# Kernel tuning notes

Hardware: AMD Instinct MI355X
Metric: run time of the kernel (lower is better)

Reference implementation:

```python
import jax, jax.numpy as jnp
import numpy as np

N_NODES = 100000
N_EDGES = 3200000
IN_FEATS = 256
N_HIDDEN = 256
N_CLASSES = 40


def setup_inputs() -> dict:
    key = jax.random.key(0)
    ks = jax.random.split(key, 8)
    features = jax.random.normal(ks[0], (N_NODES, IN_FEATS), dtype=jnp.float32)
    src = jax.random.randint(ks[1], (N_EDGES,), 0, N_NODES, dtype=jnp.int64)
    dst = jax.random.randint(ks[2], (N_EDGES,), 0, N_NODES, dtype=jnp.int64)
    # Glorot-ish init scaled down for stability
    W0 = jax.random.normal(ks[3], (IN_FEATS, N_HIDDEN), dtype=jnp.float32) * (1.0 / np.sqrt(IN_FEATS))
    W1 = jax.random.normal(ks[4], (N_HIDDEN, N_HIDDEN), dtype=jnp.float32) * (1.0 / np.sqrt(N_HIDDEN))
    W2 = jax.random.normal(ks[5], (N_HIDDEN, N_CLASSES), dtype=jnp.float32) * (1.0 / np.sqrt(N_HIDDEN))
    b0 = jnp.zeros((N_HIDDEN,), jnp.float32)
    b1 = jnp.zeros((N_HIDDEN,), jnp.float32)
    b2 = jnp.zeros((N_CLASSES,), jnp.float32)
    return {"features": features, "src": src, "dst": dst,
            "W0": W0, "b0": b0, "W1": W1, "b1": b1, "W2": W2, "b2": b2}


def _degree_norms(src, dst, n_nodes):
    ones = jnp.ones(src.shape[0], jnp.float32)
    deg_out = jax.ops.segment_sum(ones, src, num_segments=n_nodes)
    deg_in = jax.ops.segment_sum(ones, dst, num_segments=n_nodes)
    # DGL norm='both': clamp degree to >=1 before rsqrt
    norm_out = jax.lax.rsqrt(jnp.maximum(deg_out, 1.0))  # applied on source side
    norm_in = jax.lax.rsqrt(jnp.maximum(deg_in, 1.0))    # applied on dest side
    return norm_out, norm_in


def _graph_conv(h, src, dst, norm_out, norm_in, W, b, activation):
    # h: [N, Fin]. norm='both': D_in^{-1/2} * A * (D_out^{-1/2} * h) @ W + b
    in_f, out_f = W.shape
    h = h * norm_out[:, None]
    if in_f > out_f:
        # mult weight first to reduce message width (DGL optimization, same math)
        h = h @ W
        agg = jax.ops.segment_sum(h[src], dst, num_segments=h.shape[0])
    else:
        agg = jax.ops.segment_sum(h[src], dst, num_segments=h.shape[0])
        agg = agg @ W
    out = agg * norm_in[:, None] + b
    if activation is not None:
        out = activation(out)
    return out


def reference(features, src, dst, W0, b0, W1, b1, W2, b2):
    n = features.shape[0]
    norm_out, norm_in = _degree_norms(src, dst, n)
    h = _graph_conv(features, src, dst, norm_out, norm_in, W0, b0, jax.nn.relu)
    h = _graph_conv(h, src, dst, norm_out, norm_in, W1, b1, jax.nn.relu)
    h = _graph_conv(h, src, dst, norm_out, norm_in, W2, b2, None)
    return h
```

## Files before the change

### kernel.cpp

```cpp
#include <hip/hip_runtime.h>

#define NN 100000
#define NE 3200000
#define F 256
#define NCLS 40
#define NC 391
#define NBLK_H 256
#define EPB (NE / NBLK_H)
#define CW 25000

using h4 = __attribute__((ext_vector_type(4))) _Float16;
using h8 = __attribute__((ext_vector_type(8))) _Float16;
using f4 = __attribute__((ext_vector_type(4))) float;

__global__ __launch_bounds__(256) void hist_k(const int* __restrict__ src,
                                              const int* __restrict__ dst,
                                              unsigned* __restrict__ pcnt,
                                              unsigned* __restrict__ pcc) {
    __shared__ unsigned hsrc[CW];
    __shared__ unsigned hc[NC];
    int t = threadIdx.x, b = blockIdx.x;
    for (int i = t; i < CW; i += 256) hsrc[i] = 0;
    for (int i = t; i < NC; i += 256) hc[i] = 0;
    __syncthreads();
    int beg = b * EPB, end = beg + EPB;
    for (int e = beg + t; e < end; e += 256) {
        int s = src[e];
        atomicAdd(&hsrc[s >> 2], 1u << (8 * (s & 3)));
        atomicAdd(&hc[dst[e] >> 8], 1u);
    }
    __syncthreads();
    unsigned* pc = pcnt + (size_t)b * CW;
    for (int i = t; i < CW; i += 256) pc[i] = hsrc[i];
    unsigned* pb = pcc + (size_t)b * NC;
    for (int i = t; i < NC; i += 256) pb[i] = hc[i];
}

__global__ void rednout_k(const unsigned* __restrict__ pcnt, float* __restrict__ nout) {
    int w = blockIdx.x * blockDim.x + threadIdx.x;
    if (w >= CW) return;
    unsigned s0 = 0, s1 = 0, s2 = 0, s3 = 0;
    for (int b = 0; b < NBLK_H; b++) {
        unsigned v = pcnt[(size_t)b * CW + w];
        s0 += v & 255u; s1 += (v >> 8) & 255u; s2 += (v >> 16) & 255u; s3 += v >> 24;
    }
    float4 o;
    o.x = rsqrtf(fmaxf((float)s0, 1.f));
    o.y = rsqrtf(fmaxf((float)s1, 1.f));
    o.z = rsqrtf(fmaxf((float)s2, 1.f));
    o.w = rsqrtf(fmaxf((float)s3, 1.f));
    *(float4*)(nout + w * 4) = o;
}

__global__ __launch_bounds__(256) void offsets_k(const unsigned* __restrict__ pcc,
                                                 unsigned* __restrict__ curoff,
                                                 unsigned* __restrict__ totals) {
    __shared__ unsigned sh[256];
    int c = blockIdx.x, t = threadIdx.x;
    unsigned v = pcc[(size_t)t * NC + c];
    sh[t] = v;
    __syncthreads();
    for (int off = 1; off < 256; off <<= 1) {
        unsigned x = (t >= off) ? sh[t - off] : 0;
        __syncthreads();
        sh[t] += x;
        __syncthreads();
    }
    curoff[(size_t)t * NC + c] = sh[t] - v;
    if (t == 255) totals[c] = sh[255];
}

__global__ __launch_bounds__(512) void base_k(const unsigned* __restrict__ totals,
                                              int* __restrict__ cbase) {
    __shared__ unsigned sh[512];
    int t = threadIdx.x;
    unsigned v = (t < NC) ? totals[t] : 0;
    sh[t] = v;
    __syncthreads();
    for (int off = 1; off < 512; off <<= 1) {
        unsigned x = (t >= off) ? sh[t - off] : 0;
        __syncthreads();
        sh[t] += x;
        __syncthreads();
    }
    if (t < NC) cbase[t] = (int)(sh[t] - v);
    if (t == 0) cbase[NC] = NE;
}

__global__ __launch_bounds__(256) void p1scat_k(const int* __restrict__ src,
                                                const int* __restrict__ dst,
                                                const int* __restrict__ cbase,
                                                const unsigned* __restrict__ curoff,
                                                unsigned* __restrict__ ebuf) {
    __shared__ int cur[NC];
    int t = threadIdx.x, b = blockIdx.x;
    for (int i = t; i < NC; i += 256)
        cur[i] = cbase[i] + (int)curoff[(size_t)b * NC + i];
    __syncthreads();
    int beg = b * EPB, end = beg + EPB;
    for (int e = beg + t; e < end; e += 256) {
        int d = dst[e];
        int p = atomicAdd(&cur[d >> 8], 1);
        ebuf[p] = (unsigned)src[e] | ((unsigned)(d & 255) << 17);
    }
}

__global__ __launch_bounds__(256) void p2build_k(const int* __restrict__ cbase,
                                                 const unsigned* __restrict__ ebuf,
                                                 int* __restrict__ csr_src,
                                                 int* __restrict__ row_ptr,
                                                 float* __restrict__ nin) {
    __shared__ int cnt[256], cur[256], sh[256];
    int c = blockIdx.x, t = threadIdx.x;
    int beg = cbase[c], end = cbase[c + 1];
    cnt[t] = 0;
    __syncthreads();
    for (int e = beg + t; e < end; e += 256)
        atomicAdd(&cnt[(ebuf[e] >> 17) & 255], 1);
    __syncthreads();
    int v = cnt[t];
    sh[t] = v;
    __syncthreads();
    for (int off = 1; off < 256; off <<= 1) {
        int x = (t >= off) ? sh[t - off] : 0;
        __syncthreads();
        sh[t] += x;
        __syncthreads();
    }
    int pref = sh[t] - v;
    int node = c * 256 + t;
    if (node <= NN) row_ptr[node] = beg + pref;
    if (node < NN)  nin[node] = rsqrtf(fmaxf((float)v, 1.f));
    cur[t] = pref;
    __syncthreads();
    for (int e = beg + t; e < end; e += 256) {
        unsigned w = ebuf[e];
        int p = atomicAdd(&cur[(w >> 17) & 255], 1);
        csr_src[beg + p] = (int)(w & 0x1FFFFu);
    }
}

__global__ void convfeat_k(const float4* __restrict__ fin, const float* __restrict__ nout,
                           h4* __restrict__ fout, int n4) {
    int i = blockIdx.x * blockDim.x + threadIdx.x;
    if (i < n4) {
        float s = nout[i >> 6];
        float4 v = fin[i];
        h4 o;
        o[0] = (_Float16)(v.x * s);
        o[1] = (_Float16)(v.y * s);
        o[2] = (_Float16)(v.z * s);
        o[3] = (_Float16)(v.w * s);
        fout[i] = o;
    }
}

__global__ void convw_k(const float* __restrict__ W, _Float16* __restrict__ Wt,
                        int ncin, int npad) {
    int i = blockIdx.x * blockDim.x + threadIdx.x;
    if (i < npad * 256) {
        int n = i >> 8, k = i & 255;
        Wt[i] = (n < ncin) ? (_Float16)W[k * ncin + n] : (_Float16)0.0f;
    }
}

__global__ __launch_bounds__(256) void agg256h_k(
        const int* __restrict__ row_ptr, const int* __restrict__ csr_src,
        const _Float16* __restrict__ h, _Float16* __restrict__ agg, int nN) {
    int node = (blockIdx.x * blockDim.x + threadIdx.x) >> 6;
    int lane = threadIdx.x & 63;
    if (node >= nN) return;
    int half = lane >> 5, col = lane & 31;
    int beg = row_ptr[node], end = row_ptr[node + 1];
    f4 a[4][2];
#pragma unroll
    for (int u = 0; u < 4; u++) { a[u][0] = (f4){0,0,0,0}; a[u][1] = (f4){0,0,0,0}; }
    int e = beg;
    for (; e + 7 < end; e += 8) {
        int s[4];
#pragma unroll
        for (int u = 0; u < 4; u++) s[u] = csr_src[e + 2 * u + half];
        h8 v[4];
#pragma unroll
        for (int u = 0; u < 4; u++)
            v[u] = *(const h8*)(h + (size_t)s[u] * F + col * 8);
#pragma unroll
        for (int u = 0; u < 4; u++)
#pragma unroll
            for (int j = 0; j < 8; j++) a[u][j >> 2][j & 3] += (float)v[u][j];
    }
    for (int t = e + half; t < end; t += 2) {
        h8 v = *(const h8*)(h + (size_t)csr_src[t] * F + col * 8);
#pragma unroll
        for (int j = 0; j < 8; j++) a[0][j >> 2][j & 3] += (float)v[j];
    }
    float r[8];
#pragma unroll
    for (int j = 0; j < 8; j++)
        r[j] = (a[0][j >> 2][j & 3] + a[1][j >> 2][j & 3])
             + (a[2][j >> 2][j & 3] + a[3][j >> 2][j & 3]);
#pragma unroll
    for (int j = 0; j < 8; j++) r[j] += __shfl_xor(r[j], 32);
    if (half == 0) {
        h8 o;
#pragma unroll
        for (int j = 0; j < 8; j++) o[j] = (_Float16)r[j];
        *(h8*)(agg + (size_t)node * F + col * 8) = o;
    }
}

__global__ __launch_bounds__(256) void agg64h_k(
        const int* __restrict__ row_ptr, const int* __restrict__ csr_src,
        const _Float16* __restrict__ t3, const float* __restrict__ nin,
        const float* __restrict__ b2, float* __restrict__ out, int nN) {
    int node = (blockIdx.x * blockDim.x + threadIdx.x) >> 6;
    int lane = threadIdx.x & 63;
    if (node >= nN) return;
    int q = lane >> 4, c = lane & 15;
    int beg = row_ptr[node], end = row_ptr[node + 1];
    f4 a0 = {0,0,0,0}, a1 = {0,0,0,0};
    int e = beg;
    for (; e + 7 < end; e += 8) {
        int s0 = csr_src[e + q], s1 = csr_src[e + 4 + q];
        h4 v0 = *(const h4*)(t3 + (size_t)s0 * 64 + c * 4);
        h4 v1 = *(const h4*)(t3 + (size_t)s1 * 64 + c * 4);
#pragma unroll
        for (int j = 0; j < 4; j++) { a0[j] += (float)v0[j]; a1[j] += (float)v1[j]; }
    }
    for (int t = e + q; t < end; t += 4) {
        h4 v = *(const h4*)(t3 + (size_t)csr_src[t] * 64 + c * 4);
#pragma unroll
        for (int j = 0; j < 4; j++) a0[j] += (float)v[j];
    }
    float r[4];
#pragma unroll
    for (int j = 0; j < 4; j++) {
        r[j] = a0[j] + a1[j];
        r[j] += __shfl_xor(r[j], 16);
        r[j] += __shfl_xor(r[j], 32);
    }
    if (lane < 10) {
        float ni = nin[node];
        float4 o;
        o.x = r[0] * ni + b2[lane * 4 + 0];
        o.y = r[1] * ni + b2[lane * 4 + 1];
        o.z = r[2] * ni + b2[lane * 4 + 2];
        o.w = r[3] * ni + b2[lane * 4 + 3];
        *(float4*)(out + (size_t)node * NCLS + lane * 4) = o;
    }
}

template <int NT, int EPI>
__global__ __launch_bounds__(512) void gemm_lds_k(
        const _Float16* __restrict__ A, const _Float16* __restrict__ Wt,
        _Float16* __restrict__ C, int M,
        const float* __restrict__ nin, const float* __restrict__ nout,
        const float* __restrict__ bias) {
    constexpr int COLS = NT * 16;
    __shared__ _Float16 lds[COLS * 256];
    char* ldsb = (char*)lds;

    const int tid  = threadIdx.x;
    const int lane = tid & 63;
    const int w    = tid >> 6;
    const int row0 = blockIdx.x * 128;

#pragma unroll
    for (int i = 0; i < COLS / 16; i++) {
        int idx  = (i * 512 + tid) * 8;
        int byte = idx * 2;
        int row  = byte >> 9;
        int swz  = byte ^ ((row & 7) << 4);
        h8 v = *(const h8*)(Wt + idx);
        *(h8*)(ldsb + swz) = v;
    }

    int arow = row0 + w * 16 + (lane & 15);
    if (arow >= M) arow = M - 1;
    const _Float16* Ap = A + (size_t)arow * 256 + (lane >> 4) * 8;
    h8 areg[8];
#pragma unroll
    for (int i = 0; i < 8; i++) areg[i] = *(const h8*)(Ap + i * 32);

    __syncthreads();

    f4 acc[NT];
#pragma unroll
    for (int n = 0; n < NT; n++) acc[n] = (f4){0.f, 0.f, 0.f, 0.f};

#pragma unroll
    for (int k0 = 0; k0 < 8; k0++) {
        int kb = (k0 * 32 + (lane >> 4) * 8) * 2;
#pragma unroll
        for (int n = 0; n < NT; n++) {
            int r    = n * 16 + (lane & 15);
            int byte = r * 512 + kb;
            int swz  = byte ^ ((r & 7) << 4);
            h8 bf = *(const h8*)(ldsb + swz);
            acc[n] = __builtin_amdgcn_mfma_f32_16x16x32_f16(areg[k0], bf, acc[n], 0, 0, 0);
        }
    }

    __syncthreads();

    const int g  = lane >> 4;
    const int rb = row0 + w * 16 + g * 4;
    float si[4], so[4];
    if (EPI) {
#pragma unroll
        for (int r = 0; r < 4; r++) {
            int rr = rb + r; if (rr >= M) rr = M - 1;
            si[r] = nin[rr];
            so[r] = nout[rr];
        }
    }
    char* warea = ldsb + w * (16 * COLS * 2);
#pragma unroll
    for (int n = 0; n < NT; n++) {
        float bb = EPI ? bias[n * 16 + (lane & 15)] : 0.f;
#pragma unroll
        for (int r = 0; r < 4; r++) {
            float x = acc[n][r];
            if (EPI) x = fmaxf(x * si[r] + bb, 0.f) * so[r];
            int lrow = g * 4 + r;
            int lcol = n * 16 + (lane & 15);
            *(_Float16*)(warea + (size_t)(lrow * COLS + lcol) * 2) = (_Float16)x;
        }
    }

    _Float16* Crow = C + (size_t)(row0 + w * 16) * COLS;
#pragma unroll
    for (int i = 0; i < COLS / 32; i++) {
        int off  = i * 1024 + lane * 16;
        int lrow = off / (COLS * 2);
        int grow = row0 + w * 16 + lrow;
        h8 v = *(const h8*)(warea + off);
        if (grow < M) *(h8*)((char*)Crow + off) = v;
    }
}

extern "C" void kernel_launch(void* const* d_in, const int* in_sizes, int n_in,
                              void* d_out, int out_size, void* d_ws, size_t ws_size,
                              hipStream_t stream) {
    const float* features = (const float*)d_in[0];
    const int*   src      = (const int*)d_in[1];
    const int*   dst      = (const int*)d_in[2];
    const float* W0       = (const float*)d_in[3];
    const float* b0       = (const float*)d_in[4];
    const float* W1       = (const float*)d_in[5];
    const float* b1       = (const float*)d_in[6];
    const float* W2       = (const float*)d_in[7];
    const float* b2       = (const float*)d_in[8];
    float* out = (float*)d_out;

    char* ws = (char*)d_ws;
    const size_t H_BYTES = (size_t)NN * F * 2;
    _Float16* hA   = (_Float16*)(ws);
    _Float16* hB   = (_Float16*)(ws + H_BYTES);
    _Float16* t3h  = (_Float16*)(ws + 2 * H_BYTES);
    char* q = ws + 2 * H_BYTES + (size_t)NN * 64 * 2;
    int* csr_src    = (int*)q;               q += (size_t)NE * 4;
    unsigned* ebuf  = (unsigned*)q;          q += (size_t)NE * 4;
    unsigned* pcnt  = (unsigned*)q;          q += (size_t)NBLK_H * CW * 4;
    unsigned* pcc   = (unsigned*)q;          q += (size_t)NBLK_H * NC * 4 + 1024;
    unsigned* curoff= (unsigned*)q;          q += (size_t)NBLK_H * NC * 4 + 1024;
    char* p = q;
    const size_t SB = 401408;
    unsigned* totals = (unsigned*)(p + 0 * SB);
    int*   cbase   = (int*)(p + 1 * SB);
    int*   row_ptr = (int*)(p + 2 * SB);
    float* nout    = (float*)(p + 3 * SB);
    float* nin     = (float*)(p + 4 * SB);
    _Float16* Wt0  = (_Float16*)(p + 5 * SB);
    _Float16* Wt1  = (_Float16*)(p + 5 * SB + 131072);
    _Float16* Wt2  = (_Float16*)(p + 5 * SB + 262144);

    const int AGG_BLOCKS = (NN * 64 + 255) / 256;
    const int GB = (NN + 127) / 128;

    hist_k<<<NBLK_H, 256, 0, stream>>>(src, dst, pcnt, pcc);
    rednout_k<<<(CW + 255) / 256, 256, 0, stream>>>(pcnt, nout);
    offsets_k<<<NC, 256, 0, stream>>>(pcc, curoff, totals);
    base_k<<<1, 512, 0, stream>>>(totals, cbase);
    p1scat_k<<<NBLK_H, 256, 0, stream>>>(src, dst, cbase, curoff, ebuf);
    p2build_k<<<NC, 256, 0, stream>>>(cbase, ebuf, csr_src, row_ptr, nin);

    int n4 = NN * 64;
    convfeat_k<<<(n4 + 255) / 256, 256, 0, stream>>>((const float4*)features, nout,
                                                     (h4*)hB, n4);
    convw_k<<<256, 256, 0, stream>>>(W0, Wt0, 256, 256);
    convw_k<<<256, 256, 0, stream>>>(W1, Wt1, 256, 256);
    convw_k<<<64, 256, 0, stream>>>(W2, Wt2, NCLS, 64);

    agg256h_k<<<AGG_BLOCKS, 256, 0, stream>>>(row_ptr, csr_src, hB, hA, NN);
    gemm_lds_k<16, 1><<<GB, 512, 0, stream>>>(hA, Wt0, hB, NN, nin, nout, b0);

    agg256h_k<<<AGG_BLOCKS, 256, 0, stream>>>(row_ptr, csr_src, hB, hA, NN);
    gemm_lds_k<16, 1><<<GB, 512, 0, stream>>>(hA, Wt1, hB, NN, nin, nout, b1);

    gemm_lds_k<4, 0><<<GB, 512, 0, stream>>>(hB, Wt2, t3h, NN, nullptr, nullptr, nullptr);
    agg64h_k<<<AGG_BLOCKS, 256, 0, stream>>>(row_ptr, csr_src, t3h, nin, b2, out, NN);
}
```

Baseline: 918.0 us.

## Fuse layer-2 aggregation, layer-2 GEMM and layer-3 GEMM into one kernel

```diff
diff --git a/kernel.cpp b/kernel.cpp
--- a/kernel.cpp
+++ b/kernel.cpp
@@ -336,6 +336,187 @@
         int grow = row0 + w * 16 + lrow;
         h8 v = *(const h8*)(warea + off);
         if (grow < M) *(h8*)((char*)Crow + off) = v;
+    }
+}
+
+__global__ __launch_bounds__(512) void fused12_k(
+        const int* __restrict__ row_ptr, const int* __restrict__ csr_src,
+        const _Float16* __restrict__ hsrc,
+        const _Float16* __restrict__ Wt1, const _Float16* __restrict__ Wt2,
+        _Float16* __restrict__ t3, const float* __restrict__ nin,
+        const float* __restrict__ nout, const float* __restrict__ bias) {
+    __shared__ _Float16 htile[128 * 256];
+    __shared__ _Float16 wbuf[128 * 256];
+    char* hb = (char*)htile;
+    char* wb = (char*)wbuf;
+
+    const int tid  = threadIdx.x;
+    const int lane = tid & 63;
+    const int w    = tid >> 6;
+    const int row0 = blockIdx.x * 128;
+    const int half = lane >> 5, col = lane & 31;
+    const int g    = lane >> 4;
+
+    for (int n = 0; n < 16; n++) {
+        int node = row0 + w * 16 + n;
+        f4 a[4][2];
+#pragma unroll
+        for (int u = 0; u < 4; u++) { a[u][0] = (f4){0,0,0,0}; a[u][1] = (f4){0,0,0,0}; }
+        if (node < NN) {
+            int beg = row_ptr[node], end = row_ptr[node + 1];
+            int e = beg;
+            for (; e + 7 < end; e += 8) {
+                int s[4];
+#pragma unroll
+                for (int u = 0; u < 4; u++) s[u] = csr_src[e + 2 * u + half];
+                h8 v[4];
+#pragma unroll
+                for (int u = 0; u < 4; u++)
+                    v[u] = *(const h8*)(hsrc + (size_t)s[u] * F + col * 8);
+#pragma unroll
+                for (int u = 0; u < 4; u++)
+#pragma unroll
+                    for (int j = 0; j < 8; j++) a[u][j >> 2][j & 3] += (float)v[u][j];
+            }
+            for (int t = e + half; t < end; t += 2) {
+                h8 v = *(const h8*)(hsrc + (size_t)csr_src[t] * F + col * 8);
+#pragma unroll
+                for (int j = 0; j < 8; j++) a[0][j >> 2][j & 3] += (float)v[j];
+            }
+        }
+        float r[8];
+#pragma unroll
+        for (int j = 0; j < 8; j++)
+            r[j] = (a[0][j >> 2][j & 3] + a[1][j >> 2][j & 3])
+                 + (a[2][j >> 2][j & 3] + a[3][j >> 2][j & 3]);
+#pragma unroll
+        for (int j = 0; j < 8; j++) r[j] += __shfl_xor(r[j], 32);
+        if (half == 0) {
+            h8 o;
+#pragma unroll
+            for (int j = 0; j < 8; j++) o[j] = (_Float16)r[j];
+            int lr = w * 16 + n;
+            int byte = lr * 512 + col * 16;
+            *(h8*)(hb + (byte ^ ((lr & 7) << 4))) = o;
+        }
+    }
+
+    h8 areg[8];
+    {
+        int lr = w * 16 + (lane & 15);
+#pragma unroll
+        for (int k0 = 0; k0 < 8; k0++) {
+            int byte = lr * 512 + k0 * 64 + (lane >> 4) * 16;
+            areg[k0] = *(const h8*)(hb + (byte ^ ((lr & 7) << 4)));
+        }
+    }
+
+    float si[4], so[4];
+#pragma unroll
+    for (int r = 0; r < 4; r++) {
+        int rr = row0 + w * 16 + g * 4 + r; if (rr >= NN) rr = NN - 1;
+        si[r] = nin[rr]; so[r] = nout[rr];
+    }
+
+    h4 stash[2][8];
+#pragma unroll
+    for (int p = 0; p < 2; p++) {
+        if (p == 1) __syncthreads();
+#pragma unroll
+        for (int i = 0; i < 8; i++) {
+            int idx = (i * 512 + tid) * 8;
+            int byte = idx * 2;
+            int row = byte >> 9;
+            *(h8*)(wb + (byte ^ ((row & 7) << 4))) =
+                *(const h8*)(Wt1 + (size_t)p * 128 * 256 + idx);
+        }
+        __syncthreads();
+        f4 acc[8];
+#pragma unroll
+        for (int n = 0; n < 8; n++) acc[n] = (f4){0,0,0,0};
+#pragma unroll
+        for (int k0 = 0; k0 < 8; k0++) {
+            int kb = k0 * 64 + (lane >> 4) * 16;
+#pragma unroll
+            for (int n = 0; n < 8; n++) {
+                int rr = n * 16 + (lane & 15);
+                int byte = rr * 512 + kb;
+                h8 bf = *(const h8*)(wb + (byte ^ ((rr & 7) << 4)));
+                acc[n] = __builtin_amdgcn_mfma_f32_16x16x32_f16(areg[k0], bf, acc[n], 0, 0, 0);
+            }
+        }
+#pragma unroll
+        for (int n = 0; n < 8; n++) {
+            float bb = bias[p * 128 + n * 16 + (lane & 15)];
+#pragma unroll
+            for (int r = 0; r < 4; r++)
+                stash[p][n][r] = (_Float16)(fmaxf(acc[n][r] * si[r] + bb, 0.f) * so[r]);
+        }
+    }
+    __syncthreads();
+
+#pragma unroll
+    for (int p = 0; p < 2; p++)
+#pragma unroll
+        for (int n = 0; n < 8; n++)
+#pragma unroll
+            for (int r = 0; r < 4; r++) {
+                int lr = w * 16 + g * 4 + r;
+                int c = p * 128 + n * 16 + (lane & 15);
+                int byte = lr * 512 + c * 2;
+                *(_Float16*)(wb + (byte ^ ((lr & 7) << 4))) = stash[p][n][r];
+            }
+#pragma unroll
+    for (int i = 0; i < 4; i++) {
+        int idx = (i * 512 + tid) * 8;
+        int byte = idx * 2;
+        int row = byte >> 9;
+        *(h8*)(hb + (byte ^ ((row & 7) << 4))) = *(const h8*)(Wt2 + idx);
+    }
+    __syncthreads();
+
+    h8 areg2[8];
+    {
+        int lr = w * 16 + (lane & 15);
+#pragma unroll
+        for (int k0 = 0; k0 < 8; k0++) {
+            int byte = lr * 512 + k0 * 64 + (lane >> 4) * 16;
+            areg2[k0] = *(const h8*)(wb + (byte ^ ((lr & 7) << 4)));
+        }
+    }
+    f4 acc2[4];
+#pragma unroll
+    for (int n = 0; n < 4; n++) acc2[n] = (f4){0,0,0,0};
+#pragma unroll
+    for (int k0 = 0; k0 < 8; k0++) {
+        int kb = k0 * 64 + (lane >> 4) * 16;
+#pragma unroll
+        for (int n = 0; n < 4; n++) {
+            int rr = n * 16 + (lane & 15);
+            int byte = rr * 512 + kb;
+            h8 bf = *(const h8*)(hb + (byte ^ ((rr & 7) << 4)));
+            acc2[n] = __builtin_amdgcn_mfma_f32_16x16x32_f16(areg2[k0], bf, acc2[n], 0, 0, 0);
+        }
+    }
+    char* tb = hb + 32768;
+#pragma unroll
+    for (int n = 0; n < 4; n++)
+#pragma unroll
+        for (int r = 0; r < 4; r++) {
+            int lr = w * 16 + g * 4 + r;
+            int c = n * 16 + (lane & 15);
+            int byte = lr * 128 + c * 2;
+            *(_Float16*)(tb + (byte ^ ((lr & 7) << 4))) = (_Float16)acc2[n][r];
+        }
+    __syncthreads();
+#pragma unroll
+    for (int i = 0; i < 2; i++) {
+        int off = i * 8192 + tid * 16;
+        int lr = off >> 7;
+        h8 v = *(const h8*)(tb + (off ^ ((lr & 7) << 4)));
+        int grow = row0 + lr;
+        if (grow < NN)
+            *(h8*)((char*)t3 + (size_t)grow * 128 + (off & 127)) = v;
     }
 }
 
@@ -395,9 +576,8 @@
     agg256h_k<<<AGG_BLOCKS, 256, 0, stream>>>(row_ptr, csr_src, hB, hA, NN);
     gemm_lds_k<16, 1><<<GB, 512, 0, stream>>>(hA, Wt0, hB, NN, nin, nout, b0);
 
-    agg256h_k<<<AGG_BLOCKS, 256, 0, stream>>>(row_ptr, csr_src, hB, hA, NN);
-    gemm_lds_k<16, 1><<<GB, 512, 0, stream>>>(hA, Wt1, hB, NN, nin, nout, b1);
-
-    gemm_lds_k<4, 0><<<GB, 512, 0, stream>>>(hB, Wt2, t3h, NN, nullptr, nullptr, nullptr);
+    fused12_k<<<GB, 512, 0, stream>>>(row_ptr, csr_src, hB, Wt1, Wt2, t3h,
+                                      nin, nout, b1);
+
     agg64h_k<<<AGG_BLOCKS, 256, 0, stream>>>(row_ptr, csr_src, t3h, nin, b2, out, NN);
 }
```

Result: slower. 996.2 us (+8.5%).

## Use 1024-thread GEMM blocks, split degree reduction, and merge weight conversions

Applied to the files above, without the earlier changes.

```diff
diff --git a/kernel.cpp b/kernel.cpp
--- a/kernel.cpp
+++ b/kernel.cpp
@@ -36,19 +36,33 @@
     for (int i = t; i < NC; i += 256) pb[i] = hc[i];
 }
 
-__global__ void rednout_k(const unsigned* __restrict__ pcnt, float* __restrict__ nout) {
+__global__ __launch_bounds__(256) void redA_k(const unsigned* __restrict__ pcnt,
+                                              unsigned* __restrict__ cntlo,
+                                              unsigned* __restrict__ cnthi) {
+    int w = blockIdx.x * 256 + threadIdx.x;
+    if (w >= CW) return;
+    int g = blockIdx.y;
+    unsigned lo = 0, hi = 0;
+    for (int b = g * 32; b < g * 32 + 32; b++) {
+        unsigned v = pcnt[(size_t)b * CW + w];
+        lo += (v & 255u) | (((v >> 8) & 255u) << 16);
+        hi += ((v >> 16) & 255u) | ((v >> 24) << 16);
+    }
+    atomicAdd(&cntlo[w], lo);
+    atomicAdd(&cnthi[w], hi);
+}
+
+__global__ void nout2_k(const unsigned* __restrict__ cntlo,
+                        const unsigned* __restrict__ cnthi,
+                        float* __restrict__ nout) {
     int w = blockIdx.x * blockDim.x + threadIdx.x;
     if (w >= CW) return;
-    unsigned s0 = 0, s1 = 0, s2 = 0, s3 = 0;
-    for (int b = 0; b < NBLK_H; b++) {
-        unsigned v = pcnt[(size_t)b * CW + w];
-        s0 += v & 255u; s1 += (v >> 8) & 255u; s2 += (v >> 16) & 255u; s3 += v >> 24;
-    }
+    unsigned lo = cntlo[w], hi = cnthi[w];
     float4 o;
-    o.x = rsqrtf(fmaxf((float)s0, 1.f));
-    o.y = rsqrtf(fmaxf((float)s1, 1.f));
-    o.z = rsqrtf(fmaxf((float)s2, 1.f));
-    o.w = rsqrtf(fmaxf((float)s3, 1.f));
+    o.x = rsqrtf(fmaxf((float)(lo & 0xFFFFu), 1.f));
+    o.y = rsqrtf(fmaxf((float)(lo >> 16), 1.f));
+    o.z = rsqrtf(fmaxf((float)(hi & 0xFFFFu), 1.f));
+    o.w = rsqrtf(fmaxf((float)(hi >> 16), 1.f));
     *(float4*)(nout + w * 4) = o;
 }
 
@@ -155,12 +169,22 @@
     }
 }
 
-__global__ void convw_k(const float* __restrict__ W, _Float16* __restrict__ Wt,
-                        int ncin, int npad) {
+__global__ void convw_all_k(const float* __restrict__ W0, const float* __restrict__ W1,
+                            const float* __restrict__ W2,
+                            _Float16* __restrict__ Wt0, _Float16* __restrict__ Wt1,
+                            _Float16* __restrict__ Wt2) {
     int i = blockIdx.x * blockDim.x + threadIdx.x;
-    if (i < npad * 256) {
+    if (i < 65536) {
         int n = i >> 8, k = i & 255;
-        Wt[i] = (n < ncin) ? (_Float16)W[k * ncin + n] : (_Float16)0.0f;
+        Wt0[i] = (_Float16)W0[k * 256 + n];
+    } else if (i < 131072) {
+        int j = i - 65536;
+        int n = j >> 8, k = j & 255;
+        Wt1[j] = (_Float16)W1[k * 256 + n];
+    } else if (i < 147456) {
+        int j = i - 131072;
+        int n = j >> 8, k = j & 255;
+        Wt2[j] = (n < NCLS) ? (_Float16)W2[k * NCLS + n] : (_Float16)0.0f;
     }
 }
 
@@ -251,7 +275,7 @@
 }
 
 template <int NT, int EPI>
-__global__ __launch_bounds__(512) void gemm_lds_k(
+__global__ __launch_bounds__(1024) void gemm_lds_k(
         const _Float16* __restrict__ A, const _Float16* __restrict__ Wt,
         _Float16* __restrict__ C, int M,
         const float* __restrict__ nin, const float* __restrict__ nout,
@@ -263,16 +287,15 @@
     const int tid  = threadIdx.x;
     const int lane = tid & 63;
     const int w    = tid >> 6;
-    const int row0 = blockIdx.x * 128;
-
-#pragma unroll
-    for (int i = 0; i < COLS / 16; i++) {
-        int idx  = (i * 512 + tid) * 8;
+    const int row0 = blockIdx.x * 256;
+
+#pragma unroll
+    for (int i = 0; i < COLS / 32; i++) {
+        int idx  = (i * 1024 + tid) * 8;
         int byte = idx * 2;
         int row  = byte >> 9;
         int swz  = byte ^ ((row & 7) << 4);
-        h8 v = *(const h8*)(Wt + idx);
-        *(h8*)(ldsb + swz) = v;
+        *(h8*)(ldsb + swz) = *(const h8*)(Wt + idx);
     }
 
     int arow = row0 + w * 16 + (lane & 15);
@@ -371,15 +394,23 @@
     int*   row_ptr = (int*)(p + 2 * SB);
     float* nout    = (float*)(p + 3 * SB);
     float* nin     = (float*)(p + 4 * SB);
-    _Float16* Wt0  = (_Float16*)(p + 5 * SB);
-    _Float16* Wt1  = (_Float16*)(p + 5 * SB + 131072);
-    _Float16* Wt2  = (_Float16*)(p + 5 * SB + 262144);
+    unsigned* cntlo = (unsigned*)(p + 5 * SB);
+    unsigned* cnthi = (unsigned*)(p + 6 * SB);
+    _Float16* Wt0  = (_Float16*)(p + 7 * SB);
+    _Float16* Wt1  = (_Float16*)(p + 7 * SB + 131072);
+    _Float16* Wt2  = (_Float16*)(p + 7 * SB + 262144);
 
     const int AGG_BLOCKS = (NN * 64 + 255) / 256;
-    const int GB = (NN + 127) / 128;
-
+    const int GB = (NN + 255) / 256;
+
+    hipMemsetAsync(cntlo, 0, CW * 4, stream);
+    hipMemsetAsync(cnthi, 0, CW * 4, stream);
     hist_k<<<NBLK_H, 256, 0, stream>>>(src, dst, pcnt, pcc);
-    rednout_k<<<(CW + 255) / 256, 256, 0, stream>>>(pcnt, nout);
+    {
+        dim3 rg((CW + 255) / 256, 8);
+        redA_k<<<rg, 256, 0, stream>>>(pcnt, cntlo, cnthi);
+    }
+    nout2_k<<<(CW + 255) / 256, 256, 0, stream>>>(cntlo, cnthi, nout);
     offsets_k<<<NC, 256, 0, stream>>>(pcc, curoff, totals);
     base_k<<<1, 512, 0, stream>>>(totals, cbase);
     p1scat_k<<<NBLK_H, 256, 0, stream>>>(src, dst, cbase, curoff, ebuf);
@@ -388,16 +419,14 @@
     int n4 = NN * 64;
     convfeat_k<<<(n4 + 255) / 256, 256, 0, stream>>>((const float4*)features, nout,
                                                      (h4*)hB, n4);
-    convw_k<<<256, 256, 0, stream>>>(W0, Wt0, 256, 256);
-    convw_k<<<256, 256, 0, stream>>>(W1, Wt1, 256, 256);
-    convw_k<<<64, 256, 0, stream>>>(W2, Wt2, NCLS, 64);
+    convw_all_k<<<576, 256, 0, stream>>>(W0, W1, W2, Wt0, Wt1, Wt2);
 
     agg256h_k<<<AGG_BLOCKS, 256, 0, stream>>>(row_ptr, csr_src, hB, hA, NN);
-    gemm_lds_k<16, 1><<<GB, 512, 0, stream>>>(hA, Wt0, hB, NN, nin, nout, b0);
+    gemm_lds_k<16, 1><<<GB, 1024, 0, stream>>>(hA, Wt0, hB, NN, nin, nout, b0);
 
     agg256h_k<<<AGG_BLOCKS, 256, 0, stream>>>(row_ptr, csr_src, hB, hA, NN);
-    gemm_lds_k<16, 1><<<GB, 512, 0, stream>>>(hA, Wt1, hB, NN, nin, nout, b1);
-
-    gemm_lds_k<4, 0><<<GB, 512, 0, stream>>>(hB, Wt2, t3h, NN, nullptr, nullptr, nullptr);
+    gemm_lds_k<16, 1><<<GB, 1024, 0, stream>>>(hA, Wt1, hB, NN, nin, nout, b1);
+
+    gemm_lds_k<4, 0><<<GB, 1024, 0, stream>>>(hB, Wt2, t3h, NN, nullptr, nullptr, nullptr);
     agg64h_k<<<AGG_BLOCKS, 256, 0, stream>>>(row_ptr, csr_src, t3h, nin, b2, out, NN);
 }
```

New measurement: 898.8 us. -2.1%, faster.
